# Performance work log

Measured on AMD Instinct MI355X. Metric: run time of the kernel, lower is better.

## Reference

```python
import jax, jax.numpy as jnp
import numpy as np

GRID_H = 64
GRID_W = 64


def make_grid(h, w):
    # torch.meshgrid([arange(h), arange(w)], indexing='xy') -> shape (w, h);
    # grid[i, j] = (j + 0.5, i + 0.5). With h == w == 64 this is square.
    gx, gy = jnp.meshgrid(jnp.arange(h, dtype=jnp.float32),
                          jnp.arange(w, dtype=jnp.float32), indexing='xy')
    return jnp.stack([gx, gy], axis=-1) + 0.5  # (w, h, 2)


def setup_inputs() -> dict:
    key = jax.random.key(0)
    k1, k2 = jax.random.split(key)
    x = jax.random.normal(k1, (4, 128, 64, 64), dtype=jnp.float32)
    y = jax.random.normal(k2, (4, 128, 64, 64), dtype=jnp.float32)
    return {"x": x, "y": y}


def reference(x, y):
    b, c, hx, wx = x.shape
    _, _, hy, wy = y.shape
    scale = c ** (-0.5)
    grids = make_grid(GRID_H, GRID_W)[:hy, :wy].reshape(-1, 2)  # (hy*wy, 2)

    x_ = x.reshape(b, c, hx * wx)
    y_ = y.reshape(b, c, hy * wy)
    # (b, q, k) attention over all key pixels
    attn = jax.nn.softmax(jnp.einsum('bcq,bck->bqk', x_, y_) * scale, axis=-1)
    uv = jnp.einsum('bqk,kt->bqt', attn, grids)  # (b, hx*wx, 2)
    uv = uv.reshape(b, hx, wx, 2)
    # normalize to [-1, 1]
    norm = jnp.asarray([wy, hy], dtype=uv.dtype)
    uv = uv / norm * 2.0 - 1.0
    return uv
```

## Files before the change

kernel.cpp:

```cpp
#include <hip/hip_runtime.h>
#include <math.h>

typedef __attribute__((ext_vector_type(8))) _Float16 f16x8;
typedef __attribute__((ext_vector_type(4))) float f32x4;

#define NPIX 4096
#define C_DIM 128
#define SCALE2 0.12752064638518208f

#if __has_builtin(__builtin_amdgcn_exp2f)
#define EXP2(x) __builtin_amdgcn_exp2f(x)
#else
#define EXP2(x) exp2f(x)
#endif

#define WS_NEED ((size_t)4 << 20)

__global__ __launch_bounds__(256) void conv_y(const float* __restrict__ y,
                                              char* __restrict__ ws)
{
    __shared__ float T[32][132];
    const int wg  = blockIdx.x;
    const int xcd = wg & 7;
    const int b   = xcd >> 1;
    const int sl  = ((xcd & 1) << 6) | (wg >> 3);
    const int k0  = sl * 32;
    const int t   = threadIdx.x;

    {
        const int c = t >> 1, half = t & 1;
        const float* srow = y + ((size_t)b * C_DIM + c) * NPIX + k0 + half * 16;
        float4 rv[4];
        #pragma unroll
        for (int u = 0; u < 4; ++u) rv[u] = *(const float4*)(srow + u * 4);
        #pragma unroll
        for (int u = 0; u < 4; ++u) {
            T[half * 16 + u * 4 + 0][c] = rv[u].x;
            T[half * 16 + u * 4 + 1][c] = rv[u].y;
            T[half * 16 + u * 4 + 2][c] = rv[u].z;
            T[half * 16 + u * 4 + 3][c] = rv[u].w;
        }
    }
    __syncthreads();

    char* panel = ws + (size_t)b * (NPIX * 256);
    const int k = t >> 3, g2 = t & 7;
    f16x8 v0, v1;
    #pragma unroll
    for (int m = 0; m < 8; ++m) {
        v0[m] = (_Float16)T[k][g2 * 16 + m];
        v1[m] = (_Float16)T[k][g2 * 16 + 8 + m];
    }
    const int key = k0 + k, s = key & 7;
    char* drow = panel + (size_t)key * 256;
    *(f16x8*)(drow + (((2 * g2)     ^ s) << 4)) = v0;
    *(f16x8*)(drow + (((2 * g2 + 1) ^ s) << 4)) = v1;
}

__global__ __launch_bounds__(512) void uv_main(const char* __restrict__ ws,
                                               const float* __restrict__ x,
                                               float* __restrict__ out)
{
    __shared__ __align__(16) char Ys[3][32768];

    const int t = threadIdx.x, w = t >> 6, l = t & 63;
    const int n16 = l & 15, quad = l >> 4;
    const int wg  = blockIdx.x;
    const int xcd = wg & 7;
    const int b   = xcd >> 1;
    const int qt  = ((xcd & 1) << 5) | (wg >> 3);
    const int q0  = qt * 64;

    f16x8 bx[4][4];
    {
        const float* xq = x + (size_t)b * C_DIM * NPIX + q0 + n16;
        #pragma unroll
        for (int cc = 0; cc < 4; ++cc)
            #pragma unroll
            for (int qg = 0; qg < 4; ++qg) {
                f16x8 hh;
                #pragma unroll
                for (int j = 0; j < 8; ++j)
                    hh[j] = (_Float16)(xq[(size_t)(cc * 32 + quad * 8 + j) * NPIX + qg * 16] * SCALE2);
                bx[cc][qg] = hh;
            }
    }

    const char* panel = ws + (size_t)b * (NPIX * 256);

    const int arow = w * 16 + n16;
    int aoff[4];
    #pragma unroll
    for (int cc = 0; cc < 4; ++cc)
        aoff[cc] = arow * 256 + (((cc * 4 + quad) ^ (n16 & 7)) << 4);

    int soff[4];
    #pragma unroll
    for (int i = 0; i < 4; ++i) soff[i] = (w * 16 + i * 4) * 256 + l * 16;

    #pragma unroll
    for (int pb = 0; pb < 2; ++pb) {
        const char* gt = panel + (size_t)pb * 32768;
        #pragma unroll
        for (int i = 0; i < 4; ++i)
            __builtin_amdgcn_global_load_lds(
                (const __attribute__((address_space(1))) void*)(gt + soff[i]),
                (__attribute__((address_space(3))) void*)(&Ys[pb][soff[i]]), 16, 0, 0);
    }

    float gxv[4];
    #pragma unroll
    for (int r = 0; r < 4; ++r) gxv[r] = (float)((w & 3) * 16 + quad * 4 + r) + 0.5f;
    const float gyw = (float)(w >> 2) + 0.5f;
    float den[4] = {0.f, 0.f, 0.f, 0.f}, nu[4] = {0.f, 0.f, 0.f, 0.f}, nv[4] = {0.f, 0.f, 0.f, 0.f};

    int bufc = 0;
    for (int kt = 0; kt < 32; ++kt) {
        char* cur = Ys[bufc];

        if (kt < 30) {
            int bufn = bufc + 2; if (bufn >= 3) bufn -= 3;
            const char* gt = panel + (size_t)(kt + 2) * 32768;
            char* nb = Ys[bufn];
            #pragma unroll
            for (int i = 0; i < 4; ++i)
                __builtin_amdgcn_global_load_lds(
                    (const __attribute__((address_space(1))) void*)(gt + soff[i]),
                    (__attribute__((address_space(3))) void*)(&nb[soff[i]]), 16, 0, 0);
            __builtin_amdgcn_s_waitcnt(0x0F78);
        } else {
            __builtin_amdgcn_s_waitcnt(0x0F70);
        }

        f32x4 acc[4];
        #pragma unroll
        for (int qg = 0; qg < 4; ++qg) acc[qg] = (f32x4){0.f, 0.f, 0.f, 0.f};

        #pragma unroll
        for (int cc = 0; cc < 4; ++cc) {
            const f16x8 A = *(const f16x8*)(cur + aoff[cc]);
            #pragma unroll
            for (int qg = 0; qg < 4; ++qg)
                acc[qg] = __builtin_amdgcn_mfma_f32_16x16x32_f16(A, bx[cc][qg], acc[qg], 0, 0, 0);
        }

        const float gy = 2.0f * (float)kt + gyw;
        #pragma unroll
        for (int qg = 0; qg < 4; ++qg) {
            float ps = 0.f, pc = 0.f;
            #pragma unroll
            for (int r = 0; r < 4; ++r) {
                const float p = EXP2(acc[qg][r]);
                ps += p;
                pc += p * gxv[r];
            }
            den[qg] += ps;
            nu[qg]  += pc;
            nv[qg]  += gy * ps;
        }
        ++bufc; if (bufc >= 3) bufc -= 3;
    }

    #pragma unroll
    for (int qg = 0; qg < 4; ++qg) {
        #pragma unroll
        for (int mk = 16; mk <= 32; mk <<= 1) {
            den[qg] += __shfl_xor(den[qg], mk);
            nu[qg]  += __shfl_xor(nu[qg],  mk);
            nv[qg]  += __shfl_xor(nv[qg],  mk);
        }
    }
    __syncthreads();
    float* red = (float*)&Ys[0][0];
    if (quad == 0) {
        #pragma unroll
        for (int qg = 0; qg < 4; ++qg) {
            const int base = (w * 64 + qg * 16 + n16) * 3;
            red[base + 0] = den[qg];
            red[base + 1] = nu[qg];
            red[base + 2] = nv[qg];
        }
    }
    __syncthreads();
    if (t < 64) {
        float d = 0.f, u = 0.f, v = 0.f;
        #pragma unroll
        for (int ww = 0; ww < 8; ++ww) {
            d += red[(ww * 64 + t) * 3 + 0];
            u += red[(ww * 64 + t) * 3 + 1];
            v += red[(ww * 64 + t) * 3 + 2];
        }
        const float inv = 1.0f / d;
        *(float2*)(out + ((size_t)b * NPIX + q0 + t) * 2) =
            make_float2(u * inv * 0.03125f - 1.0f, v * inv * 0.03125f - 1.0f);
    }
}

__global__ __launch_bounds__(256, 2) void uv_attn_kernel(
    const float* __restrict__ x, const float* __restrict__ y, float* __restrict__ out)
{
    __shared__ float Xs[C_DIM][32];
    __shared__ float Ysf[64][128];
    const float SCALE = 0.08838834764831845f;
    const int tid = threadIdx.x;
    const int wgid = blockIdx.x;
    const int xcd = wgid & 7;
    const int b = xcd & 3;
    const int q0 = (((xcd >> 2) << 6) | (wgid >> 3)) * 32;
    const float* xb = x + (size_t)b * C_DIM * NPIX + q0;
    {
        const int cr = tid >> 3;
        const int cc = (tid & 7) << 2;
        #pragma unroll
        for (int i = 0; i < 4; ++i) {
            float4 v = *(const float4*)(xb + (size_t)(cr + (i << 5)) * NPIX + cc);
            v.x *= SCALE; v.y *= SCALE; v.z *= SCALE; v.w *= SCALE;
            *(float4*)(&Xs[cr + (i << 5)][cc]) = v;
        }
    }
    const int rg = tid >> 4;
    const int lane16 = tid & 15;
    const int r0 = rg << 1;
    const int col0 = lane16 << 3;
    float gxv[8];
    #pragma unroll
    for (int j2 = 0; j2 < 8; ++j2) gxv[j2] = (float)((col0 & 63) + j2) + 0.5f;
    const float gyb = (float)(lane16 >> 3) + 0.5f;
    float m_run[2] = {-INFINITY, -INFINITY};
    float den[2] = {0.f, 0.f}, nu[2] = {0.f, 0.f}, nv[2] = {0.f, 0.f};
    const int yr = tid >> 5;
    const int yc = (tid & 31) << 2;
    const float* ybase = y + (size_t)b * C_DIM * NPIX;
    for (int kt = 0; kt < 32; ++kt) {
        float S[2][8];
        #pragma unroll
        for (int r = 0; r < 2; ++r)
            #pragma unroll
            for (int j2 = 0; j2 < 8; ++j2) S[r][j2] = 0.f;
        #pragma unroll
        for (int cb = 0; cb < 2; ++cb) {
            __syncthreads();
            const float* yt = ybase + (size_t)(cb << 6) * NPIX + kt * 128;
            #pragma unroll
            for (int i = 0; i < 8; ++i)
                *(float4*)(&Ysf[yr + (i << 3)][yc]) =
                    *(const float4*)(yt + (size_t)(yr + (i << 3)) * NPIX + yc);
            __syncthreads();
            const int cbase = cb << 6;
            #pragma unroll 16
            for (int c = 0; c < 64; ++c) {
                const float2 xa = *(const float2*)(&Xs[cbase + c][r0]);
                const float4 ya = *(const float4*)(&Ysf[c][col0]);
                const float4 yb4 = *(const float4*)(&Ysf[c][col0 + 4]);
                S[0][0] += xa.x * ya.x;  S[0][1] += xa.x * ya.y;
                S[0][2] += xa.x * ya.z;  S[0][3] += xa.x * ya.w;
                S[0][4] += xa.x * yb4.x; S[0][5] += xa.x * yb4.y;
                S[0][6] += xa.x * yb4.z; S[0][7] += xa.x * yb4.w;
                S[1][0] += xa.y * ya.x;  S[1][1] += xa.y * ya.y;
                S[1][2] += xa.y * ya.z;  S[1][3] += xa.y * ya.w;
                S[1][4] += xa.y * yb4.x; S[1][5] += xa.y * yb4.y;
                S[1][6] += xa.y * yb4.z; S[1][7] += xa.y * yb4.w;
            }
        }
        const float gy = gyb + 2.0f * (float)kt;
        #pragma unroll
        for (int r = 0; r < 2; ++r) {
            float tmax = S[r][0];
            #pragma unroll
            for (int j2 = 1; j2 < 8; ++j2) tmax = fmaxf(tmax, S[r][j2]);
            #pragma unroll
            for (int mk = 8; mk >= 1; mk >>= 1) tmax = fmaxf(tmax, __shfl_xor(tmax, mk, 16));
            const float mnew = fmaxf(m_run[r], tmax);
            const float alpha = __expf(m_run[r] - mnew);
            m_run[r] = mnew;
            float psum = 0.f, pu = 0.f;
            #pragma unroll
            for (int j2 = 0; j2 < 8; ++j2) {
                const float p = __expf(S[r][j2] - mnew);
                psum += p; pu += p * gxv[j2];
            }
            den[r] = den[r] * alpha + psum;
            nu[r] = nu[r] * alpha + pu;
            nv[r] = nv[r] * alpha + gy * psum;
        }
    }
    #pragma unroll
    for (int r = 0; r < 2; ++r)
        #pragma unroll
        for (int mk = 8; mk >= 1; mk >>= 1) {
            den[r] += __shfl_xor(den[r], mk, 16);
            nu[r] += __shfl_xor(nu[r], mk, 16);
            nv[r] += __shfl_xor(nv[r], mk, 16);
        }
    if (lane16 == 0) {
        #pragma unroll
        for (int r = 0; r < 2; ++r) {
            const float inv = 1.0f / den[r];
            const int q = q0 + r0 + r;
            *(float2*)(out + ((size_t)b * NPIX + q) * 2) =
                make_float2(nu[r] * inv * 0.03125f - 1.0f, nv[r] * inv * 0.03125f - 1.0f);
        }
    }
}

extern "C" void kernel_launch(void* const* d_in, const int* in_sizes, int n_in,
                              void* d_out, int out_size, void* d_ws, size_t ws_size,
                              hipStream_t stream) {
    const float* x = (const float*)d_in[0];
    const float* y = (const float*)d_in[1];
    float* out = (float*)d_out;
    if (ws_size >= WS_NEED) {
        hipLaunchKernelGGL(conv_y, dim3(512), dim3(256), 0, stream, y, (char*)d_ws);
        hipLaunchKernelGGL(uv_main, dim3(256), dim3(512), 0, stream,
                           (const char*)d_ws, x, out);
    } else {
        hipLaunchKernelGGL(uv_attn_kernel, dim3(512), dim3(256), 0, stream, x, y, out);
    }
}
```

Measured before the change: 91.51 us.

## Fuse Y fp16 conversion into main kernel with register double-buffered loads

Drops the separate conv_y pre-pass and the workspace panel. The fused kernel reads fp32 Y directly from global memory into registers (strided scalar loads, double-buffered across key tiles) and converts it to fp16 just before the MFMA, replacing the LDS triple buffer. This removes one kernel launch and the workspace round trip. In exchange, each of the 64 query-tile workgroups per batch re-reads the full fp32 Y (double the bytes of fp16) with uncoalesced per-channel scalar loads and repeats the conversion, which raises global and L2 traffic.

```diff
diff --git a/kernel.cpp b/kernel.cpp
--- a/kernel.cpp
+++ b/kernel.cpp
@@ -14,54 +14,11 @@
 #define EXP2(x) exp2f(x)
 #endif
 
-#define WS_NEED ((size_t)4 << 20)
-
-__global__ __launch_bounds__(256) void conv_y(const float* __restrict__ y,
-                                              char* __restrict__ ws)
+__global__ __launch_bounds__(512, 2) void uv_fused(const float* __restrict__ x,
+                                                   const float* __restrict__ y,
+                                                   float* __restrict__ out)
 {
-    __shared__ float T[32][132];
-    const int wg  = blockIdx.x;
-    const int xcd = wg & 7;
-    const int b   = xcd >> 1;
-    const int sl  = ((xcd & 1) << 6) | (wg >> 3);
-    const int k0  = sl * 32;
-    const int t   = threadIdx.x;
-
-    {
-        const int c = t >> 1, half = t & 1;
-        const float* srow = y + ((size_t)b * C_DIM + c) * NPIX + k0 + half * 16;
-        float4 rv[4];
-        #pragma unroll
-        for (int u = 0; u < 4; ++u) rv[u] = *(const float4*)(srow + u * 4);
-        #pragma unroll
-        for (int u = 0; u < 4; ++u) {
-            T[half * 16 + u * 4 + 0][c] = rv[u].x;
-            T[half * 16 + u * 4 + 1][c] = rv[u].y;
-            T[half * 16 + u * 4 + 2][c] = rv[u].z;
-            T[half * 16 + u * 4 + 3][c] = rv[u].w;
-        }
-    }
-    __syncthreads();
-
-    char* panel = ws + (size_t)b * (NPIX * 256);
-    const int k = t >> 3, g2 = t & 7;
-    f16x8 v0, v1;
-    #pragma unroll
-    for (int m = 0; m < 8; ++m) {
-        v0[m] = (_Float16)T[k][g2 * 16 + m];
-        v1[m] = (_Float16)T[k][g2 * 16 + 8 + m];
-    }
-    const int key = k0 + k, s = key & 7;
-    char* drow = panel + (size_t)key * 256;
-    *(f16x8*)(drow + (((2 * g2)     ^ s) << 4)) = v0;
-    *(f16x8*)(drow + (((2 * g2 + 1) ^ s) << 4)) = v1;
-}
-
-__global__ __launch_bounds__(512) void uv_main(const char* __restrict__ ws,
-                                               const float* __restrict__ x,
-                                               float* __restrict__ out)
-{
-    __shared__ __align__(16) char Ys[3][32768];
+    __shared__ float red[8][64][3];
 
     const int t = threadIdx.x, w = t >> 6, l = t & 63;
     const int n16 = l & 15, quad = l >> 4;
@@ -86,27 +43,7 @@
             }
     }
 
-    const char* panel = ws + (size_t)b * (NPIX * 256);
-
-    const int arow = w * 16 + n16;
-    int aoff[4];
-    #pragma unroll
-    for (int cc = 0; cc < 4; ++cc)
-        aoff[cc] = arow * 256 + (((cc * 4 + quad) ^ (n16 & 7)) << 4);
-
-    int soff[4];
-    #pragma unroll
-    for (int i = 0; i < 4; ++i) soff[i] = (w * 16 + i * 4) * 256 + l * 16;
-
-    #pragma unroll
-    for (int pb = 0; pb < 2; ++pb) {
-        const char* gt = panel + (size_t)pb * 32768;
-        #pragma unroll
-        for (int i = 0; i < 4; ++i)
-            __builtin_amdgcn_global_load_lds(
-                (const __attribute__((address_space(1))) void*)(gt + soff[i]),
-                (__attribute__((address_space(3))) void*)(&Ys[pb][soff[i]]), 16, 0, 0);
-    }
+    const float* yq = y + ((size_t)b * C_DIM + quad * 8) * NPIX + w * 16 + n16;
 
     float gxv[4];
     #pragma unroll
@@ -114,52 +51,57 @@
     const float gyw = (float)(w >> 2) + 0.5f;
     float den[4] = {0.f, 0.f, 0.f, 0.f}, nu[4] = {0.f, 0.f, 0.f, 0.f}, nv[4] = {0.f, 0.f, 0.f, 0.f};
 
-    int bufc = 0;
-    for (int kt = 0; kt < 32; ++kt) {
-        char* cur = Ys[bufc];
+    float fA[4][8], fB[4][8];
 
-        if (kt < 30) {
-            int bufn = bufc + 2; if (bufn >= 3) bufn -= 3;
-            const char* gt = panel + (size_t)(kt + 2) * 32768;
-            char* nb = Ys[bufn];
-            #pragma unroll
-            for (int i = 0; i < 4; ++i)
-                __builtin_amdgcn_global_load_lds(
-                    (const __attribute__((address_space(1))) void*)(gt + soff[i]),
-                    (__attribute__((address_space(3))) void*)(&nb[soff[i]]), 16, 0, 0);
-            __builtin_amdgcn_s_waitcnt(0x0F78);
-        } else {
-            __builtin_amdgcn_s_waitcnt(0x0F70);
-        }
+#define LOADT(BUF, KT) do {                                                     \
+    const unsigned kof_ = (unsigned)(KT) * 128u;                                \
+    _Pragma("unroll")                                                           \
+    for (int cc_ = 0; cc_ < 4; ++cc_) {                                         \
+        _Pragma("unroll")                                                       \
+        for (int j_ = 0; j_ < 8; ++j_)                                          \
+            BUF[cc_][j_] = yq[(unsigned)((cc_ * 32 + j_) * NPIX) + kof_];       \
+    } } while (0)
 
-        f32x4 acc[4];
-        #pragma unroll
-        for (int qg = 0; qg < 4; ++qg) acc[qg] = (f32x4){0.f, 0.f, 0.f, 0.f};
+#define BODY(KT, CUR) do {                                                      \
+    f32x4 acc_[4];                                                              \
+    _Pragma("unroll")                                                           \
+    for (int qg_ = 0; qg_ < 4; ++qg_) acc_[qg_] = (f32x4){0.f, 0.f, 0.f, 0.f};  \
+    _Pragma("unroll")                                                           \
+    for (int cc_ = 0; cc_ < 4; ++cc_) {                                         \
+        f16x8 A_;                                                               \
+        _Pragma("unroll")                                                       \
+        for (int j_ = 0; j_ < 8; ++j_) A_[j_] = (_Float16)CUR[cc_][j_];         \
+        _Pragma("unroll")                                                       \
+        for (int qg_ = 0; qg_ < 4; ++qg_)                                       \
+            acc_[qg_] = __builtin_amdgcn_mfma_f32_16x16x32_f16(A_, bx[cc_][qg_], acc_[qg_], 0, 0, 0); \
+    }                                                                           \
+    const float gy_ = 2.0f * (float)(KT) + gyw;                                 \
+    _Pragma("unroll")                                                           \
+    for (int qg_ = 0; qg_ < 4; ++qg_) {                                         \
+        float ps_ = 0.f, pc_ = 0.f;                                             \
+        _Pragma("unroll")                                                       \
+        for (int r_ = 0; r_ < 4; ++r_) {                                        \
+            const float p_ = EXP2(acc_[qg_][r_]);                               \
+            ps_ += p_;                                                          \
+            pc_ += p_ * gxv[r_];                                                \
+        }                                                                       \
+        den[qg_] += ps_;                                                        \
+        nu[qg_]  += pc_;                                                        \
+        nv[qg_]  += gy_ * ps_;                                                  \
+    } } while (0)
 
-        #pragma unroll
-        for (int cc = 0; cc < 4; ++cc) {
-            const f16x8 A = *(const f16x8*)(cur + aoff[cc]);
-            #pragma unroll
-            for (int qg = 0; qg < 4; ++qg)
-                acc[qg] = __builtin_amdgcn_mfma_f32_16x16x32_f16(A, bx[cc][qg], acc[qg], 0, 0, 0);
-        }
+    LOADT(fA, 0);
+    #pragma unroll 1
+    for (int kt2 = 0; kt2 < 16; ++kt2) {
+        const int kte = 2 * kt2;
+        LOADT(fB, kte + 1);
+        BODY(kte, fA);
+        if (kt2 < 15) LOADT(fA, kte + 2);
+        BODY(kte + 1, fB);
+    }
 
-        const float gy = 2.0f * (float)kt + gyw;
-        #pragma unroll
-        for (int qg = 0; qg < 4; ++qg) {
-            float ps = 0.f, pc = 0.f;
-            #pragma unroll
-            for (int r = 0; r < 4; ++r) {
-                const float p = EXP2(acc[qg][r]);
-                ps += p;
-                pc += p * gxv[r];
-            }
-            den[qg] += ps;
-            nu[qg]  += pc;
-            nv[qg]  += gy * ps;
-        }
-        ++bufc; if (bufc >= 3) bufc -= 3;
-    }
+#undef LOADT
+#undef BODY
 
     #pragma unroll
     for (int qg = 0; qg < 4; ++qg) {
@@ -170,15 +112,12 @@
             nv[qg]  += __shfl_xor(nv[qg],  mk);
         }
     }
-    __syncthreads();
-    float* red = (float*)&Ys[0][0];
     if (quad == 0) {
         #pragma unroll
         for (int qg = 0; qg < 4; ++qg) {
-            const int base = (w * 64 + qg * 16 + n16) * 3;
-            red[base + 0] = den[qg];
-            red[base + 1] = nu[qg];
-            red[base + 2] = nv[qg];
+            red[w][qg * 16 + n16][0] = den[qg];
+            red[w][qg * 16 + n16][1] = nu[qg];
+            red[w][qg * 16 + n16][2] = nv[qg];
         }
     }
     __syncthreads();
@@ -186,9 +125,9 @@
         float d = 0.f, u = 0.f, v = 0.f;
         #pragma unroll
         for (int ww = 0; ww < 8; ++ww) {
-            d += red[(ww * 64 + t) * 3 + 0];
-            u += red[(ww * 64 + t) * 3 + 1];
-            v += red[(ww * 64 + t) * 3 + 2];
+            d += red[ww][t][0];
+            u += red[ww][t][1];
+            v += red[ww][t][2];
         }
         const float inv = 1.0f / d;
         *(float2*)(out + ((size_t)b * NPIX + q0 + t) * 2) =
@@ -196,124 +135,10 @@
     }
 }
 
-__global__ __launch_bounds__(256, 2) void uv_attn_kernel(
-    const float* __restrict__ x, const float* __restrict__ y, float* __restrict__ out)
-{
-    __shared__ float Xs[C_DIM][32];
-    __shared__ float Ysf[64][128];
-    const float SCALE = 0.08838834764831845f;
-    const int tid = threadIdx.x;
-    const int wgid = blockIdx.x;
-    const int xcd = wgid & 7;
-    const int b = xcd & 3;
-    const int q0 = (((xcd >> 2) << 6) | (wgid >> 3)) * 32;
-    const float* xb = x + (size_t)b * C_DIM * NPIX + q0;
-    {
-        const int cr = tid >> 3;
-        const int cc = (tid & 7) << 2;
-        #pragma unroll
-        for (int i = 0; i < 4; ++i) {
-            float4 v = *(const float4*)(xb + (size_t)(cr + (i << 5)) * NPIX + cc);
-            v.x *= SCALE; v.y *= SCALE; v.z *= SCALE; v.w *= SCALE;
-            *(float4*)(&Xs[cr + (i << 5)][cc]) = v;
-        }
-    }
-    const int rg = tid >> 4;
-    const int lane16 = tid & 15;
-    const int r0 = rg << 1;
-    const int col0 = lane16 << 3;
-    float gxv[8];
-    #pragma unroll
-    for (int j2 = 0; j2 < 8; ++j2) gxv[j2] = (float)((col0 & 63) + j2) + 0.5f;
-    const float gyb = (float)(lane16 >> 3) + 0.5f;
-    float m_run[2] = {-INFINITY, -INFINITY};
-    float den[2] = {0.f, 0.f}, nu[2] = {0.f, 0.f}, nv[2] = {0.f, 0.f};
-    const int yr = tid >> 5;
-    const int yc = (tid & 31) << 2;
-    const float* ybase = y + (size_t)b * C_DIM * NPIX;
-    for (int kt = 0; kt < 32; ++kt) {
-        float S[2][8];
-        #pragma unroll
-        for (int r = 0; r < 2; ++r)
-            #pragma unroll
-            for (int j2 = 0; j2 < 8; ++j2) S[r][j2] = 0.f;
-        #pragma unroll
-        for (int cb = 0; cb < 2; ++cb) {
-            __syncthreads();
-            const float* yt = ybase + (size_t)(cb << 6) * NPIX + kt * 128;
-            #pragma unroll
-            for (int i = 0; i < 8; ++i)
-                *(float4*)(&Ysf[yr + (i << 3)][yc]) =
-                    *(const float4*)(yt + (size_t)(yr + (i << 3)) * NPIX + yc);
-            __syncthreads();
-            const int cbase = cb << 6;
-            #pragma unroll 16
-            for (int c = 0; c < 64; ++c) {
-                const float2 xa = *(const float2*)(&Xs[cbase + c][r0]);
-                const float4 ya = *(const float4*)(&Ysf[c][col0]);
-                const float4 yb4 = *(const float4*)(&Ysf[c][col0 + 4]);
-                S[0][0] += xa.x * ya.x;  S[0][1] += xa.x * ya.y;
-                S[0][2] += xa.x * ya.z;  S[0][3] += xa.x * ya.w;
-                S[0][4] += xa.x * yb4.x; S[0][5] += xa.x * yb4.y;
-                S[0][6] += xa.x * yb4.z; S[0][7] += xa.x * yb4.w;
-                S[1][0] += xa.y * ya.x;  S[1][1] += xa.y * ya.y;
-                S[1][2] += xa.y * ya.z;  S[1][3] += xa.y * ya.w;
-                S[1][4] += xa.y * yb4.x; S[1][5] += xa.y * yb4.y;
-                S[1][6] += xa.y * yb4.z; S[1][7] += xa.y * yb4.w;
-            }
-        }
-        const float gy = gyb + 2.0f * (float)kt;
-        #pragma unroll
-        for (int r = 0; r < 2; ++r) {
-            float tmax = S[r][0];
-            #pragma unroll
-            for (int j2 = 1; j2 < 8; ++j2) tmax = fmaxf(tmax, S[r][j2]);
-            #pragma unroll
-            for (int mk = 8; mk >= 1; mk >>= 1) tmax = fmaxf(tmax, __shfl_xor(tmax, mk, 16));
-            const float mnew = fmaxf(m_run[r], tmax);
-            const float alpha = __expf(m_run[r] - mnew);
-            m_run[r] = mnew;
-            float psum = 0.f, pu = 0.f;
-            #pragma unroll
-            for (int j2 = 0; j2 < 8; ++j2) {
-                const float p = __expf(S[r][j2] - mnew);
-                psum += p; pu += p * gxv[j2];
-            }
-            den[r] = den[r] * alpha + psum;
-            nu[r] = nu[r] * alpha + pu;
-            nv[r] = nv[r] * alpha + gy * psum;
-        }
-    }
-    #pragma unroll
-    for (int r = 0; r < 2; ++r)
-        #pragma unroll
-        for (int mk = 8; mk >= 1; mk >>= 1) {
-            den[r] += __shfl_xor(den[r], mk, 16);
-            nu[r] += __shfl_xor(nu[r], mk, 16);
-            nv[r] += __shfl_xor(nv[r], mk, 16);
-        }
-    if (lane16 == 0) {
-        #pragma unroll
-        for (int r = 0; r < 2; ++r) {
-            const float inv = 1.0f / den[r];
-            const int q = q0 + r0 + r;
-            *(float2*)(out + ((size_t)b * NPIX + q) * 2) =
-                make_float2(nu[r] * inv * 0.03125f - 1.0f, nv[r] * inv * 0.03125f - 1.0f);
-        }
-    }
-}
-
 extern "C" void kernel_launch(void* const* d_in, const int* in_sizes, int n_in,
                               void* d_out, int out_size, void* d_ws, size_t ws_size,
                               hipStream_t stream) {
-    const float* x = (const float*)d_in[0];
-    const float* y = (const float*)d_in[1];
-    float* out = (float*)d_out;
-    if (ws_size >= WS_NEED) {
-        hipLaunchKernelGGL(conv_y, dim3(512), dim3(256), 0, stream, y, (char*)d_ws);
-        hipLaunchKernelGGL(uv_main, dim3(256), dim3(512), 0, stream,
-                           (const char*)d_ws, x, out);
-    } else {
-        hipLaunchKernelGGL(uv_attn_kernel, dim3(512), dim3(256), 0, stream, x, y, out);
-    }
+    (void)in_sizes; (void)n_in; (void)out_size; (void)d_ws; (void)ws_size;
+    hipLaunchKernelGGL(uv_fused, dim3(256), dim3(512), 0, stream,
+                       (const float*)d_in[0], (const float*)d_in[1], (float*)d_out);
 }
```

New measurement: 99.33 us. 8.5% more time.

## Load key tiles straight to registers and double the waves per block

Applied to the files above, without the earlier changes.

The main attention kernel drops its triple-buffered LDS staging of the f16 key panel, which used async global-to-LDS copies. Each wave now reads its MFMA A operands directly from global memory into registers, with a two-deep register prefetch. The block grows from 512 to 1024 threads (16 waves), so each wave covers 16 key tiles instead of 32, and the final cross-wave reduction is widened to match. This removes LDS traffic and waitcnt stalls. In exchange, loads become uncoalesced row-strided 16-byte global reads that rely on L2, and register pressure rises under the 1024-thread launch bound.

```diff
diff --git a/kernel.cpp b/kernel.cpp
--- a/kernel.cpp
+++ b/kernel.cpp
@@ -57,11 +57,11 @@
     *(f16x8*)(drow + (((2 * g2 + 1) ^ s) << 4)) = v1;
 }
 
-__global__ __launch_bounds__(512) void uv_main(const char* __restrict__ ws,
-                                               const float* __restrict__ x,
-                                               float* __restrict__ out)
+__global__ __launch_bounds__(1024) void uv_main(const char* __restrict__ ws,
+                                                const float* __restrict__ x,
+                                                float* __restrict__ out)
 {
-    __shared__ __align__(16) char Ys[3][32768];
+    __shared__ float red[16][64][3];
 
     const int t = threadIdx.x, w = t >> 6, l = t & 63;
     const int n16 = l & 15, quad = l >> 4;
@@ -87,26 +87,11 @@
     }
 
     const char* panel = ws + (size_t)b * (NPIX * 256);
-
-    const int arow = w * 16 + n16;
-    int aoff[4];
+    const char* yrow  = panel + (size_t)(w * 16 + n16) * 256;
+    int goff[4];
     #pragma unroll
     for (int cc = 0; cc < 4; ++cc)
-        aoff[cc] = arow * 256 + (((cc * 4 + quad) ^ (n16 & 7)) << 4);
-
-    int soff[4];
-    #pragma unroll
-    for (int i = 0; i < 4; ++i) soff[i] = (w * 16 + i * 4) * 256 + l * 16;
-
-    #pragma unroll
-    for (int pb = 0; pb < 2; ++pb) {
-        const char* gt = panel + (size_t)pb * 32768;
-        #pragma unroll
-        for (int i = 0; i < 4; ++i)
-            __builtin_amdgcn_global_load_lds(
-                (const __attribute__((address_space(1))) void*)(gt + soff[i]),
-                (__attribute__((address_space(3))) void*)(&Ys[pb][soff[i]]), 16, 0, 0);
-    }
+        goff[cc] = ((cc * 4 + quad) ^ (n16 & 7)) << 4;
 
     float gxv[4];
     #pragma unroll
@@ -114,52 +99,52 @@
     const float gyw = (float)(w >> 2) + 0.5f;
     float den[4] = {0.f, 0.f, 0.f, 0.f}, nu[4] = {0.f, 0.f, 0.f, 0.f}, nv[4] = {0.f, 0.f, 0.f, 0.f};
 
-    int bufc = 0;
-    for (int kt = 0; kt < 32; ++kt) {
-        char* cur = Ys[bufc];
-
-        if (kt < 30) {
-            int bufn = bufc + 2; if (bufn >= 3) bufn -= 3;
-            const char* gt = panel + (size_t)(kt + 2) * 32768;
-            char* nb = Ys[bufn];
-            #pragma unroll
-            for (int i = 0; i < 4; ++i)
-                __builtin_amdgcn_global_load_lds(
-                    (const __attribute__((address_space(1))) void*)(gt + soff[i]),
-                    (__attribute__((address_space(3))) void*)(&nb[soff[i]]), 16, 0, 0);
-            __builtin_amdgcn_s_waitcnt(0x0F78);
-        } else {
-            __builtin_amdgcn_s_waitcnt(0x0F70);
-        }
-
-        f32x4 acc[4];
-        #pragma unroll
-        for (int qg = 0; qg < 4; ++qg) acc[qg] = (f32x4){0.f, 0.f, 0.f, 0.f};
-
-        #pragma unroll
-        for (int cc = 0; cc < 4; ++cc) {
-            const f16x8 A = *(const f16x8*)(cur + aoff[cc]);
-            #pragma unroll
-            for (int qg = 0; qg < 4; ++qg)
-                acc[qg] = __builtin_amdgcn_mfma_f32_16x16x32_f16(A, bx[cc][qg], acc[qg], 0, 0, 0);
-        }
-
-        const float gy = 2.0f * (float)kt + gyw;
-        #pragma unroll
-        for (int qg = 0; qg < 4; ++qg) {
-            float ps = 0.f, pc = 0.f;
-            #pragma unroll
-            for (int r = 0; r < 4; ++r) {
-                const float p = EXP2(acc[qg][r]);
-                ps += p;
-                pc += p * gxv[r];
-            }
-            den[qg] += ps;
-            nu[qg]  += pc;
-            nv[qg]  += gy * ps;
-        }
-        ++bufc; if (bufc >= 3) bufc -= 3;
-    }
+    f16x8 aA[4], aB[4];
+
+#define LOADA(BUF, KT) do {                                                     \
+    const char* rp_ = yrow + (size_t)(KT) * 65536;                              \
+    _Pragma("unroll")                                                           \
+    for (int cc_ = 0; cc_ < 4; ++cc_)                                           \
+        BUF[cc_] = *(const f16x8*)(rp_ + goff[cc_]);                            \
+    } while (0)
+
+#define BODY(KT, CUR) do {                                                      \
+    f32x4 acc_[4];                                                              \
+    _Pragma("unroll")                                                           \
+    for (int qg_ = 0; qg_ < 4; ++qg_) acc_[qg_] = (f32x4){0.f, 0.f, 0.f, 0.f};  \
+    _Pragma("unroll")                                                           \
+    for (int cc_ = 0; cc_ < 4; ++cc_) {                                         \
+        _Pragma("unroll")                                                       \
+        for (int qg_ = 0; qg_ < 4; ++qg_)                                       \
+            acc_[qg_] = __builtin_amdgcn_mfma_f32_16x16x32_f16(CUR[cc_], bx[cc_][qg_], acc_[qg_], 0, 0, 0); \
+    }                                                                           \
+    const float gy_ = 4.0f * (float)(KT) + gyw;                                 \
+    _Pragma("unroll")                                                           \
+    for (int qg_ = 0; qg_ < 4; ++qg_) {                                         \
+        float ps_ = 0.f, pc_ = 0.f;                                             \
+        _Pragma("unroll")                                                       \
+        for (int r_ = 0; r_ < 4; ++r_) {                                        \
+            const float p_ = EXP2(acc_[qg_][r_]);                               \
+            ps_ += p_;                                                          \
+            pc_ += p_ * gxv[r_];                                                \
+        }                                                                       \
+        den[qg_] += ps_;                                                        \
+        nu[qg_]  += pc_;                                                        \
+        nv[qg_]  += gy_ * ps_;                                                  \
+    } } while (0)
+
+    LOADA(aA, 0);
+    #pragma unroll 1
+    for (int kt2 = 0; kt2 < 8; ++kt2) {
+        const int kte = 2 * kt2;
+        LOADA(aB, kte + 1);
+        BODY(kte, aA);
+        if (kt2 < 7) LOADA(aA, kte + 2);
+        BODY(kte + 1, aB);
+    }
+
+#undef LOADA
+#undef BODY
 
     #pragma unroll
     for (int qg = 0; qg < 4; ++qg) {
@@ -170,25 +155,22 @@
             nv[qg]  += __shfl_xor(nv[qg],  mk);
         }
     }
-    __syncthreads();
-    float* red = (float*)&Ys[0][0];
     if (quad == 0) {
         #pragma unroll
         for (int qg = 0; qg < 4; ++qg) {
-            const int base = (w * 64 + qg * 16 + n16) * 3;
-            red[base + 0] = den[qg];
-            red[base + 1] = nu[qg];
-            red[base + 2] = nv[qg];
+            red[w][qg * 16 + n16][0] = den[qg];
+            red[w][qg * 16 + n16][1] = nu[qg];
+            red[w][qg * 16 + n16][2] = nv[qg];
         }
     }
     __syncthreads();
     if (t < 64) {
         float d = 0.f, u = 0.f, v = 0.f;
         #pragma unroll
-        for (int ww = 0; ww < 8; ++ww) {
-            d += red[(ww * 64 + t) * 3 + 0];
-            u += red[(ww * 64 + t) * 3 + 1];
-            v += red[(ww * 64 + t) * 3 + 2];
+        for (int ww = 0; ww < 16; ++ww) {
+            d += red[ww][t][0];
+            u += red[ww][t][1];
+            v += red[ww][t][2];
         }
         const float inv = 1.0f / d;
         *(float2*)(out + ((size_t)b * NPIX + q0 + t) * 2) =
@@ -311,7 +293,7 @@
     float* out = (float*)d_out;
     if (ws_size >= WS_NEED) {
         hipLaunchKernelGGL(conv_y, dim3(512), dim3(256), 0, stream, y, (char*)d_ws);
-        hipLaunchKernelGGL(uv_main, dim3(256), dim3(512), 0, stream,
+        hipLaunchKernelGGL(uv_main, dim3(256), dim3(1024), 0, stream,
                            (const char*)d_ws, x, out);
     } else {
         hipLaunchKernelGGL(uv_attn_kernel, dim3(512), dim3(256), 0, stream, x, y, out);
```

Result: slower. 152.0 us (+66.1%).

## Halve query tile per block, double grid, switch to double-buffered key panels

Applied to the files above, without the earlier changes.

Each uv_main block now handles 32 queries instead of 64, and the grid doubles to 512 blocks so more CUs and waves are busy. The key-panel ring drops from three LDS buffers to two, with a matching waitcnt change. A dedicated reduction array replaces reuse of the panel buffer, and launch bounds request 4 blocks per CU. This trades higher occupancy and parallelism for twice the total key-panel traffic from L2, since each block streams the whole 1 MB panel for fewer queries, and for a shallower prefetch depth.

```diff
diff --git a/kernel.cpp b/kernel.cpp
--- a/kernel.cpp
+++ b/kernel.cpp
@@ -57,27 +57,40 @@
     *(f16x8*)(drow + (((2 * g2 + 1) ^ s) << 4)) = v1;
 }
 
-__global__ __launch_bounds__(512) void uv_main(const char* __restrict__ ws,
-                                               const float* __restrict__ x,
-                                               float* __restrict__ out)
+__global__ __launch_bounds__(512, 4) void uv_main(const char* __restrict__ ws,
+                                                  const float* __restrict__ x,
+                                                  float* __restrict__ out)
 {
-    __shared__ __align__(16) char Ys[3][32768];
+    __shared__ __align__(16) char Ys[2][32768];
+    __shared__ float red[8][32][3];
 
     const int t = threadIdx.x, w = t >> 6, l = t & 63;
     const int n16 = l & 15, quad = l >> 4;
     const int wg  = blockIdx.x;
     const int xcd = wg & 7;
     const int b   = xcd >> 1;
-    const int qt  = ((xcd & 1) << 5) | (wg >> 3);
-    const int q0  = qt * 64;
-
-    f16x8 bx[4][4];
+    const int qt  = ((xcd & 1) << 6) | (wg >> 3);
+    const int q0  = qt * 32;
+
+    const char* panel = ws + (size_t)b * (NPIX * 256);
+
+    int soff[4];
+    #pragma unroll
+    for (int i = 0; i < 4; ++i) soff[i] = (w * 16 + i * 4) * 256 + l * 16;
+
+    #pragma unroll
+    for (int i = 0; i < 4; ++i)
+        __builtin_amdgcn_global_load_lds(
+            (const __attribute__((address_space(1))) void*)(panel + soff[i]),
+            (__attribute__((address_space(3))) void*)(&Ys[0][soff[i]]), 16, 0, 0);
+
+    f16x8 bx[4][2];
     {
         const float* xq = x + (size_t)b * C_DIM * NPIX + q0 + n16;
         #pragma unroll
         for (int cc = 0; cc < 4; ++cc)
             #pragma unroll
-            for (int qg = 0; qg < 4; ++qg) {
+            for (int qg = 0; qg < 2; ++qg) {
                 f16x8 hh;
                 #pragma unroll
                 for (int j = 0; j < 8; ++j)
@@ -86,67 +99,50 @@
             }
     }
 
-    const char* panel = ws + (size_t)b * (NPIX * 256);
-
     const int arow = w * 16 + n16;
     int aoff[4];
     #pragma unroll
     for (int cc = 0; cc < 4; ++cc)
         aoff[cc] = arow * 256 + (((cc * 4 + quad) ^ (n16 & 7)) << 4);
 
-    int soff[4];
-    #pragma unroll
-    for (int i = 0; i < 4; ++i) soff[i] = (w * 16 + i * 4) * 256 + l * 16;
-
-    #pragma unroll
-    for (int pb = 0; pb < 2; ++pb) {
-        const char* gt = panel + (size_t)pb * 32768;
-        #pragma unroll
-        for (int i = 0; i < 4; ++i)
-            __builtin_amdgcn_global_load_lds(
-                (const __attribute__((address_space(1))) void*)(gt + soff[i]),
-                (__attribute__((address_space(3))) void*)(&Ys[pb][soff[i]]), 16, 0, 0);
-    }
-
     float gxv[4];
     #pragma unroll
     for (int r = 0; r < 4; ++r) gxv[r] = (float)((w & 3) * 16 + quad * 4 + r) + 0.5f;
     const float gyw = (float)(w >> 2) + 0.5f;
-    float den[4] = {0.f, 0.f, 0.f, 0.f}, nu[4] = {0.f, 0.f, 0.f, 0.f}, nv[4] = {0.f, 0.f, 0.f, 0.f};
-
-    int bufc = 0;
+    float den[2] = {0.f, 0.f}, nu[2] = {0.f, 0.f}, nv[2] = {0.f, 0.f};
+
+    #pragma unroll 1
     for (int kt = 0; kt < 32; ++kt) {
-        char* cur = Ys[bufc];
-
-        if (kt < 30) {
-            int bufn = bufc + 2; if (bufn >= 3) bufn -= 3;
-            const char* gt = panel + (size_t)(kt + 2) * 32768;
-            char* nb = Ys[bufn];
+        char* cur = Ys[kt & 1];
+
+        if (kt < 31) {
+            const char* gt = panel + (size_t)(kt + 1) * 32768;
+            char* nb = Ys[(kt + 1) & 1];
             #pragma unroll
             for (int i = 0; i < 4; ++i)
                 __builtin_amdgcn_global_load_lds(
                     (const __attribute__((address_space(1))) void*)(gt + soff[i]),
                     (__attribute__((address_space(3))) void*)(&nb[soff[i]]), 16, 0, 0);
-            __builtin_amdgcn_s_waitcnt(0x0F78);
+            __builtin_amdgcn_s_waitcnt(0x0F74);
         } else {
             __builtin_amdgcn_s_waitcnt(0x0F70);
         }
 
-        f32x4 acc[4];
-        #pragma unroll
-        for (int qg = 0; qg < 4; ++qg) acc[qg] = (f32x4){0.f, 0.f, 0.f, 0.f};
+        f32x4 acc[2];
+        #pragma unroll
+        for (int qg = 0; qg < 2; ++qg) acc[qg] = (f32x4){0.f, 0.f, 0.f, 0.f};
 
         #pragma unroll
         for (int cc = 0; cc < 4; ++cc) {
             const f16x8 A = *(const f16x8*)(cur + aoff[cc]);
             #pragma unroll
-            for (int qg = 0; qg < 4; ++qg)
+            for (int qg = 0; qg < 2; ++qg)
                 acc[qg] = __builtin_amdgcn_mfma_f32_16x16x32_f16(A, bx[cc][qg], acc[qg], 0, 0, 0);
         }
 
         const float gy = 2.0f * (float)kt + gyw;
         #pragma unroll
-        for (int qg = 0; qg < 4; ++qg) {
+        for (int qg = 0; qg < 2; ++qg) {
             float ps = 0.f, pc = 0.f;
             #pragma unroll
             for (int r = 0; r < 4; ++r) {
@@ -158,11 +154,10 @@
             nu[qg]  += pc;
             nv[qg]  += gy * ps;
         }
-        ++bufc; if (bufc >= 3) bufc -= 3;
-    }
-
-    #pragma unroll
-    for (int qg = 0; qg < 4; ++qg) {
+    }
+
+    #pragma unroll
+    for (int qg = 0; qg < 2; ++qg) {
         #pragma unroll
         for (int mk = 16; mk <= 32; mk <<= 1) {
             den[qg] += __shfl_xor(den[qg], mk);
@@ -170,25 +165,22 @@
             nv[qg]  += __shfl_xor(nv[qg],  mk);
         }
     }
+    if (quad == 0) {
+        #pragma unroll
+        for (int qg = 0; qg < 2; ++qg) {
+            red[w][qg * 16 + n16][0] = den[qg];
+            red[w][qg * 16 + n16][1] = nu[qg];
+            red[w][qg * 16 + n16][2] = nv[qg];
+        }
+    }
     __syncthreads();
-    float* red = (float*)&Ys[0][0];
-    if (quad == 0) {
-        #pragma unroll
-        for (int qg = 0; qg < 4; ++qg) {
-            const int base = (w * 64 + qg * 16 + n16) * 3;
-            red[base + 0] = den[qg];
-            red[base + 1] = nu[qg];
-            red[base + 2] = nv[qg];
-        }
-    }
-    __syncthreads();
-    if (t < 64) {
+    if (t < 32) {
         float d = 0.f, u = 0.f, v = 0.f;
         #pragma unroll
         for (int ww = 0; ww < 8; ++ww) {
-            d += red[(ww * 64 + t) * 3 + 0];
-            u += red[(ww * 64 + t) * 3 + 1];
-            v += red[(ww * 64 + t) * 3 + 2];
+            d += red[ww][t][0];
+            u += red[ww][t][1];
+            v += red[ww][t][2];
         }
         const float inv = 1.0f / d;
         *(float2*)(out + ((size_t)b * NPIX + q0 + t) * 2) =
@@ -311,7 +303,7 @@
     float* out = (float*)d_out;
     if (ws_size >= WS_NEED) {
         hipLaunchKernelGGL(conv_y, dim3(512), dim3(256), 0, stream, y, (char*)d_ws);
-        hipLaunchKernelGGL(uv_main, dim3(256), dim3(512), 0, stream,
+        hipLaunchKernelGGL(uv_main, dim3(512), dim3(512), 0, stream,
                            (const char*)d_ws, x, out);
     } else {
         hipLaunchKernelGGL(uv_attn_kernel, dim3(512), dim3(256), 0, stream, x, y, out);
```

Result: slower. 95.80 us (+4.7%).
